# Optimization experiments

Hardware: AMD Instinct MI355X
Metric: run time of the kernel (lower is better)

## Reference

```python
import jax, jax.numpy as jnp
import numpy as np

N_FILTERS = 64
FILTER_SIZE = 64
N_FRAMES = 64
N_TO_KEEP = 128
MIN_SIZE = 512
N_SAMPLES = 32768
BATCH = 8


def pos_encoding(n_elements, n_sinusoids):
    t = np.linspace(1e-8, 1.0, n_elements)
    freq = np.linspace(1e-3, 1.0, n_sinusoids)
    return np.sin(t[:, None] * freq[None, :]).astype(np.float32)


def gammatone_filter_bank(n_filters, size, sr=22050.0):
    # 4th-order gammatone impulse responses, linearly spaced center freqs
    t = np.arange(size) / sr
    freqs = np.linspace(20.0, sr / 2 - 20.0, n_filters)
    b = 1.019 * 24.7 * (4.37 * freqs / 1000.0 + 1.0)  # ERB bandwidths
    g = (t[None, :] ** 3) * np.exp(-2 * np.pi * b[:, None] * t[None, :]) \
        * np.cos(2 * np.pi * freqs[:, None] * t[None, :])
    g = g / (np.abs(g).max(axis=-1, keepdims=True) + 1e-12)
    return g.astype(np.float32)


def setup_inputs() -> dict:
    key = jax.random.key(0)
    k1, k2 = jax.random.split(key)
    return {
        'target': jax.random.normal(k1, (BATCH, 1, N_SAMPLES), dtype=jnp.float32),
        'recon': jax.random.normal(k2, (BATCH, 1, N_SAMPLES), dtype=jnp.float32),
        'filters': jnp.asarray(gammatone_filter_bank(N_FILTERS, FILTER_SIZE)),
        'proj_time': jnp.asarray(pos_encoding(N_FRAMES, 128)),
        'proj_freq': jnp.asarray(pos_encoding(N_FILTERS, 128)),
    }


def fft_frequency_decompose(x, min_size):
    # band-limited octave decomposition: band of size s holds rfft bins [s/4, s/2)
    coeffs = jnp.fft.rfft(x, norm='ortho')
    n = x.shape[-1]
    bands = []
    start, end = 0, min_size // 2
    while end <= n // 2:
        spec = jnp.zeros(x.shape[:-1] + (end + 1,), dtype=coeffs.dtype)
        spec = spec.at[..., start:end].set(coeffs[..., start:end])
        bands.append(jnp.fft.irfft(spec, n=end * 2, norm='ortho'))
        start, end = end, end * 2
    return bands


def fft_convolve(a, b):
    n = a.shape[-1]
    pa = jnp.pad(a, [(0, 0)] * (a.ndim - 1) + [(0, n)])
    pb = jnp.pad(b, [(0, 0)] * (b.ndim - 1) + [(0, n)])
    spec = jnp.fft.rfft(pa) * jnp.fft.rfft(pb)  # broadcasts [B,1,.] x [1,F,.]
    return jnp.fft.irfft(spec, n=2 * n)[..., :n]


def max_pool1d(x, kernel, stride, pad):
    return jax.lax.reduce_window(
        x, -jnp.inf, jax.lax.max,
        (1, 1, kernel), (1, 1, stride),
        [(0, 0), (0, 0), (pad, pad)])


def sparsify2(x, k):
    # top-k over flattened (channels*time); pack events as value-scaled time
    # one-hots and binary channel one-hots
    b, c, t = x.shape
    flat = x.reshape(b, c * t)
    values, indices = jax.lax.top_k(flat, k)  # [b, k]
    ch, tm = indices // t, indices % t
    packed = (tm[..., None] == jnp.arange(t)[None, None, :]).astype(x.dtype) * values[..., None]  # [b,k,t]
    one_hot = (ch[..., None] == jnp.arange(c)[None, None, :]).astype(x.dtype)  # [b,k,c]
    return packed, one_hot


def _feature(x, filters, proj_time, proj_freq):
    bands = fft_frequency_decompose(x, MIN_SIZE)
    outs = []
    for band in bands:  # fixed small set of structurally distinct bands
        samples = band.shape[-1]
        filt = jnp.pad(filters[None, :, :], ((0, 0), (0, 0), (0, samples - FILTER_SIZE)))
        result = fft_convolve(band, filt)  # [B, n_filters, samples]
        stride = samples // 64
        pooled = max_pool1d(result, 2 * stride, stride, stride // 2)[..., :samples]  # [B, 64, 64]
        packed, one_hot = sparsify2(pooled, N_TO_KEEP)
        a = packed @ proj_time   # [B, k, 128]
        b = one_hot @ proj_freq  # [B, k, 128]
        outs.append(jnp.concatenate([a, b], axis=-1))
    return jnp.concatenate(outs, axis=-1)  # [B, k, 256 * n_bands]


def reference(target, recon, filters, proj_time, proj_freq):
    t = _feature(target, filters, proj_time, proj_freq)
    r = _feature(recon, filters, proj_time, proj_freq)
    return jnp.abs(t - r).mean()
```

## Files before the change

kernel.cpp:

```cpp
#include <hip/hip_runtime.h>
#include <hip/hip_bf16.h>

#define N_SAMP    32768
#define NBINS     16384
#define NSIG      16
#define NBANDS    7
#define K_TOP     128
#define BAND_STRIDE 65472

#define SST_F   0
#define SST_PT  4096
#define SST_PF  12288
#define SST_TOT 20480

#define TWO_PI 6.283185307179586f

typedef __attribute__((ext_vector_type(8))) short bf16x8;
typedef __attribute__((ext_vector_type(4))) float f32x4;

__device__ __forceinline__ float bf2f(__hip_bfloat16 v) { return __bfloat162float(v); }

__device__ __forceinline__ unsigned encf(float f) {
    unsigned u = __float_as_uint(f);
    return (u & 0x80000000u) ? ~u : (u | 0x80000000u);
}
__device__ __forceinline__ float decf(unsigned u) {
    return __uint_as_float((u & 0x80000000u) ? (u ^ 0x80000000u) : ~u);
}

__device__ __forceinline__ int band_M1sh(int b) { return b < 3 ? 4 : (b < 4 ? 5 : 6); }
__device__ __forceinline__ int band_Lsh(int b) {
    return b == 0 ? 5 : (b == 1 ? 6 : (b < 5 ? 7 : (b == 5 ? 8 : 9)));
}
__device__ __forceinline__ int band_M2sh(int b) {
    return b < 2 ? 4 : (b < 5 ? 5 : (b == 5 ? 6 : 7));
}

__global__ __launch_bounds__(256) void k_stage(
    const void* __restrict__ t, const void* __restrict__ f,
    const void* __restrict__ pt, const void* __restrict__ pf,
    __hip_bfloat16* __restrict__ staged,
    float* __restrict__ bands, float* __restrict__ accum,
    int* __restrict__ counter)
{
    const int tid = threadIdx.x;
    const int bx  = blockIdx.x;
    if (bx == SST_TOT / 256) {
        for (int i = tid; i < NSIG * 448; i += 256) {
            int sig = i / 448, rem = i - sig * 448;
            int g = rem >> 6, j = rem & 63;
            int off = 64 * g + 512 * ((1 << g) - 1);
            bands[(size_t)sig * BAND_STRIDE + off + j] = 0.f;
        }
        if (tid == 0) { accum[0] = 0.f; counter[0] = 0; }
        return;
    }
    float pv = bf2f(((const __hip_bfloat16*)t)[tid & 63]);
    int bad = (fabsf(pv) > 1e8f) || (pv != pv);
    const int isf32 = (__ballot(bad) != 0ull);
    const int id = bx * 256 + tid;
    const void* src; int idx;
    if (id < SST_PT)      { src = f;  idx = id; }
    else if (id < SST_PF) { src = pt; idx = id - SST_PT; }
    else                  { src = pf; idx = id - SST_PF; }
    float v = isf32 ? ((const float*)src)[idx]
                    : bf2f(((const __hip_bfloat16*)src)[idx]);
    staged[id] = __float2bfloat16(v);
}

__global__ __launch_bounds__(256) void k_fwd1(
    const void* __restrict__ tgt, const void* __restrict__ rec,
    float* __restrict__ T)
{
    const int tid   = threadIdx.x;
    const int sig   = blockIdx.y;
    const int nbase = (blockIdx.x & 1) * 128;
    const int kgrp  = (blockIdx.x >> 1) * 64;
    __shared__ __align__(16) __hip_bfloat16 xT[128][136];
    __shared__ float ct[128], st[128];

    if (tid < 128) {
        float sv, cv;
        sincosf(TWO_PI * (float)tid * (1.f / 128.f), &sv, &cv);
        ct[tid] = cv; st[tid] = sv;
    }

    float pv = bf2f(((const __hip_bfloat16*)tgt)[tid & 63]);
    int bad = (fabsf(pv) > 1e8f) || (pv != pv);
    const int isf32 = (__ballot(bad) != 0ull);
    const void* xsrc = (sig < 8) ? tgt : rec;
    const int soff = (sig & 7) * N_SAMP;

    const int rloc = tid & 127;
    const int chb  = (tid >> 7) * 64;
    for (int c8 = 0; c8 < 64; c8 += 8) {
        union { bf16x8 v; __hip_bfloat16 h[8]; } u;
        #pragma unroll
        for (int uu = 0; uu < 8; ++uu) {
            int n1 = chb + c8 + uu;
            int gi = soff + n1 * 256 + nbase + rloc;
            float xv = isf32 ? ((const float*)xsrc)[gi]
                             : bf2f(((const __hip_bfloat16*)xsrc)[gi]);
            u.h[uu] = __float2bfloat16(xv);
        }
        *(bf16x8*)(&xT[rloc][chb + c8]) = u.v;
    }
    __syncthreads();

    const int tl = tid & 15, quad = (tid >> 4) & 3, w = tid >> 6;
    const int k1 = kgrp + w * 16 + tl;
    bf16x8 Arh[4], Arl[4], Aih[4], Ail[4];
    #pragma unroll
    for (int ki = 0; ki < 4; ++ki) {
        union { bf16x8 v; __hip_bfloat16 h[8]; } rh, rl, ih, il;
        #pragma unroll
        for (int j = 0; j < 8; ++j) {
            int n1 = ki * 32 + quad * 8 + j;
            int tt = (k1 * n1) & 127;
            float wre = ct[tt], wim = -st[tt];
            __hip_bfloat16 h1 = __float2bfloat16(wre);
            rh.h[j] = h1;
            rl.h[j] = __float2bfloat16(wre - bf2f(h1));
            __hip_bfloat16 h2 = __float2bfloat16(wim);
            ih.h[j] = h2;
            il.h[j] = __float2bfloat16(wim - bf2f(h2));
        }
        Arh[ki] = rh.v; Arl[ki] = rl.v; Aih[ki] = ih.v; Ail[ki] = il.v;
    }

    float2* To = (float2*)T + (size_t)sig * 128 * 256;
    const int mk = kgrp + w * 16 + quad * 4;
    for (int ni = 0; ni < 8; ++ni) {
        bf16x8 B[4];
        #pragma unroll
        for (int ki = 0; ki < 4; ++ki)
            B[ki] = *(const bf16x8*)(&xT[ni * 16 + tl][ki * 32 + quad * 8]);
        f32x4 aR = {0.f,0.f,0.f,0.f}, aI = {0.f,0.f,0.f,0.f};
        #pragma unroll
        for (int ki = 0; ki < 4; ++ki) {
            aR = __builtin_amdgcn_mfma_f32_16x16x32_bf16(Arh[ki], B[ki], aR, 0, 0, 0);
            aR = __builtin_amdgcn_mfma_f32_16x16x32_bf16(Arl[ki], B[ki], aR, 0, 0, 0);
            aI = __builtin_amdgcn_mfma_f32_16x16x32_bf16(Aih[ki], B[ki], aI, 0, 0, 0);
            aI = __builtin_amdgcn_mfma_f32_16x16x32_bf16(Ail[ki], B[ki], aI, 0, 0, 0);
        }
        const int n2 = nbase + ni * 16 + tl;
        #pragma unroll
        for (int rg = 0; rg < 4; ++rg) {
            int k1e = mk + rg;
            float sv, cv;
            sincosf((TWO_PI / 32768.f) * (float)(k1e * n2), &sv, &cv);
            float Tr = aR[rg] * cv + aI[rg] * sv;
            float Ti = aI[rg] * cv - aR[rg] * sv;
            To[(size_t)k1e * 256 + n2] = make_float2(Tr, Ti);
        }
    }
}

__global__ __launch_bounds__(128) void k_fwd2(
    const float* __restrict__ T, float* __restrict__ C)
{
    const int k2  = threadIdx.x;
    const int k1  = blockIdx.x;
    const int sig = blockIdx.y;
    __shared__ float2 Ts[256];
    const float2* Tin = (const float2*)T + ((size_t)sig * 128 + k1) * 256;
    for (int i = k2; i < 256; i += 128) Ts[i] = Tin[i];
    __syncthreads();
    float er[4], ei[4];
    #pragma unroll
    for (int c = 0; c < 4; ++c) {
        float sv, cv;
        sincosf(-TWO_PI * (float)((c * k2) & 255) * (1.f / 256.f), &sv, &cv);
        er[c] = cv; ei[c] = sv;
    }
    float s4, c4;
    sincosf(-TWO_PI * (float)((4 * k2) & 255) * (1.f / 256.f), &s4, &c4);
    float Xr[4] = {0.f,0.f,0.f,0.f}, Xi[4] = {0.f,0.f,0.f,0.f};
    for (int n2 = 0; n2 < 256; n2 += 4) {
        #pragma unroll
        for (int c = 0; c < 4; ++c) {
            float2 t = Ts[n2 + c];
            Xr[c] += t.x * er[c] - t.y * ei[c];
            Xi[c] += t.x * ei[c] + t.y * er[c];
            float nr = er[c] * c4 - ei[c] * s4;
            ei[c]    = er[c] * s4 + ei[c] * c4;
            er[c] = nr;
        }
    }
    const float inv = 5.5242717280199030e-3f;
    float xr = (Xr[0] + Xr[1]) + (Xr[2] + Xr[3]);
    float xi = (Xi[0] + Xi[1]) + (Xi[2] + Xi[3]);
    float2* Co = (float2*)C + (size_t)sig * NBINS;
    Co[k1 + 128 * k2] = make_float2(xr * inv, xi * inv);
}

__global__ __launch_bounds__(256) void k_synthA(
    const float* __restrict__ C, float* __restrict__ G)
{
    const int tid = threadIdx.x;
    const int sig = blockIdx.y;
    const int bix = 63 - blockIdx.x;
    const int band = (bix == 0) ? 0 : (32 - __clz(bix));
    const int lbx  = (band == 0) ? 0 : (bix - (1 << (band - 1)));
    const int s    = 512 << band;
    const int m1sh = band_M1sh(band);
    const int lsh  = band_Lsh(band);
    const int m2sh = band_M2sh(band);
    const int M2   = 1 << m2sh;
    const int L    = 1 << lsh;
    const int L4   = L >> 2;
    const int a    = (band == 0) ? 0 : (128 << band);
    const int tix  = lbx * 256 + tid;
    const int j1lo = (lbx * 256) >> (lsh - 2);
    int j1cnt = 256 >> (lsh - 2);
    if (j1cnt > (1 << m1sh)) j1cnt = 1 << m1sh;
    __shared__ float2 Ds[256];
    const float2* D = (const float2*)C + (size_t)sig * NBINS + a;
    for (int i = tid; i < (j1cnt << m2sh); i += 256) {
        int j1o = i >> m2sh, j2 = i & (M2 - 1);
        Ds[i] = D[(j1lo + j1o) + (j2 << m1sh)];
    }
    __syncthreads();
    if (tix >= (128 << band)) return;
    const int j1o = (tix >> (lsh - 2)) - j1lo;
    const int m   = tix & (L4 - 1);
    const float2* Dj = Ds + (j1o << m2sh);
    float e0r = 1.f, e0i = 0.f, e1r, e1i, sr, si;
    sincosf(TWO_PI * (float)m / (float)L, &e1i, &e1r);
    sincosf(TWO_PI * (float)(2 * m) / (float)L, &si, &sr);
    float ar[4] = {0.f,0.f,0.f,0.f}, ai[4] = {0.f,0.f,0.f,0.f};
    for (int j2 = 0; j2 < M2; j2 += 4) {
        {   float2 d = Dj[j2];
            float tr = d.x * e0r - d.y * e0i, ti = d.x * e0i + d.y * e0r;
            ar[0] += tr; ai[0] += ti; ar[1] += tr; ai[1] += ti;
            ar[2] += tr; ai[2] += ti; ar[3] += tr; ai[3] += ti;
            float nr = e0r * sr - e0i * si; e0i = e0r * si + e0i * sr; e0r = nr;
        }
        {   float2 d = Dj[j2 + 1];
            float tr = d.x * e1r - d.y * e1i, ti = d.x * e1i + d.y * e1r;
            ar[0] += tr; ai[0] += ti;
            ar[1] -= ti; ai[1] += tr;
            ar[2] -= tr; ai[2] -= ti;
            ar[3] += ti; ai[3] -= tr;
            float nr = e1r * sr - e1i * si; e1i = e1r * si + e1i * sr; e1r = nr;
        }
        {   float2 d = Dj[j2 + 2];
            float tr = d.x * e0r - d.y * e0i, ti = d.x * e0i + d.y * e0r;
            ar[0] += tr; ai[0] += ti;
            ar[1] -= tr; ai[1] -= ti;
            ar[2] += tr; ai[2] += ti;
            ar[3] -= tr; ai[3] -= ti;
            float nr = e0r * sr - e0i * si; e0i = e0r * si + e0i * sr; e0r = nr;
        }
        {   float2 d = Dj[j2 + 3];
            float tr = d.x * e1r - d.y * e1i, ti = d.x * e1i + d.y * e1r;
            ar[0] += tr; ai[0] += ti;
            ar[1] += ti; ai[1] -= tr;
            ar[2] -= tr; ai[2] -= ti;
            ar[3] -= ti; ai[3] += tr;
            float nr = e1r * sr - e1i * si; e1i = e1r * si + e1i * sr; e1r = nr;
        }
    }
    const float sc = 2.f * rsqrtf((float)s);
    float2* Go = (float2*)G + (size_t)sig * 65024 + 512 * ((1 << band) - 1);
    const int base = ((tix >> (lsh - 2)) << lsh) + m;
    #pragma unroll
    for (int q = 0; q < 4; ++q)
        Go[base + q * L4] = make_float2(ar[q] * sc, ai[q] * sc);
}

__global__ __launch_bounds__(256) void k_synthB(
    const float* __restrict__ C, const float* __restrict__ G,
    float* __restrict__ bands)
{
    const int tid = threadIdx.x;
    const int sig = blockIdx.y;
    const int bix = 63 - blockIdx.x;
    const int band = (bix == 0) ? 0 : (32 - __clz(bix));
    const int lbx  = (band == 0) ? 0 : (bix - (1 << (band - 1)));
    const int s    = 512 << band;
    const int M1   = 1 << band_M1sh(band);
    const int lsh  = band_Lsh(band);
    const int n    = lbx * 256 + tid;
    const int s4   = s >> 2;
    if (n >= s4) return;
    const int m    = n & ((1 << lsh) - 1);
    const float2* Gi = (const float2*)G + (size_t)sig * 65024 + 512 * ((1 << band) - 1);
    float e0r = 1.f, e0i = 0.f, e1r, e1i, sr, si;
    sincosf(TWO_PI * (float)n / (float)s, &e1i, &e1r);
    sincosf(TWO_PI * (float)(2 * n) / (float)s, &si, &sr);
    float zr[4] = {0.f,0.f,0.f,0.f}, zi[4] = {0.f,0.f,0.f,0.f};
    for (int j1 = 0; j1 < M1; j1 += 4) {
        {   float2 g = Gi[((j1 + 0) << lsh) + m];
            float tr = g.x * e0r - g.y * e0i, ti = g.x * e0i + g.y * e0r;
            zr[0] += tr; zi[0] += ti; zr[1] += tr; zi[1] += ti;
            zr[2] += tr; zi[2] += ti; zr[3] += tr; zi[3] += ti;
            float nr = e0r * sr - e0i * si; e0i = e0r * si + e0i * sr; e0r = nr;
        }
        {   float2 g = Gi[((j1 + 1) << lsh) + m];
            float tr = g.x * e1r - g.y * e1i, ti = g.x * e1i + g.y * e1r;
            zr[0] += tr; zi[0] += ti;
            zr[1] -= ti; zi[1] += tr;
            zr[2] -= tr; zi[2] -= ti;
            zr[3] += ti; zi[3] -= tr;
            float nr = e1r * sr - e1i * si; e1i = e1r * si + e1i * sr; e1r = nr;
        }
        {   float2 g = Gi[((j1 + 2) << lsh) + m];
            float tr = g.x * e0r - g.y * e0i, ti = g.x * e0i + g.y * e0r;
            zr[0] += tr; zi[0] += ti;
            zr[1] -= tr; zi[1] -= ti;
            zr[2] += tr; zi[2] += ti;
            zr[3] -= tr; zi[3] -= ti;
            float nr = e0r * sr - e0i * si; e0i = e0r * si + e0i * sr; e0r = nr;
        }
        {   float2 g = Gi[((j1 + 3) << lsh) + m];
            float tr = g.x * e1r - g.y * e1i, ti = g.x * e1i + g.y * e1r;
            zr[0] += tr; zi[0] += ti;
            zr[1] += ti; zi[1] -= tr;
            zr[2] -= tr; zi[2] -= ti;
            zr[3] -= ti; zi[3] += tr;
            float nr = e1r * sr - e1i * si; e1i = e1r * si + e1i * sr; e1r = nr;
        }
    }
    const int poff = 64 * (band + 1) + 512 * ((1 << band) - 1);
    float* bo = bands + (size_t)sig * BAND_STRIDE + poff;
    if (band == 0) {
        const float dc = C[(size_t)sig * NBINS * 2] * 0.04419417382415922f;
        #pragma unroll
        for (int q = 0; q < 4; ++q) bo[n + q * s4] = zr[q] - dc;
    } else {
        #pragma unroll
        for (int q = 0; q < 4; ++q) {
            float val;
            switch (n & 3) {
                case 0:  val =  zr[q]; break;
                case 1:  val = -zi[q]; break;
                case 2:  val = -zr[q]; break;
                default: val =  zi[q]; break;
            }
            bo[n + q * s4] = val;
        }
    }
}

__global__ __launch_bounds__(256) void k_conv(
    const float* __restrict__ bands,
    const __hip_bfloat16* __restrict__ filters,
    float* __restrict__ segG)
{
    const int tid  = threadIdx.x;
    const int sig  = blockIdx.y;
    const int c    = blockIdx.x;
    const int band = 31 - __clz(c + 1);
    const int cidx = c + 1 - (1 << band);
    const int poff = 64 * (band + 1) + 512 * ((1 << band) - 1);
    const float* bp = bands + (size_t)sig * BAND_STRIDE + poff + cidx * 512;

    __shared__ __align__(16) __hip_bfloat16 xr[8][584];
    __shared__ float segP[64 * 4];

    for (int i = tid; i < 576; i += 256) {
        __hip_bfloat16 b = __float2bfloat16(bp[511 - i]);
        #pragma unroll
        for (int p = 0; p < 8; ++p) {
            int idx = i - p;
            if (idx >= 0) xr[p][idx] = b;
        }
    }
    __syncthreads();

    const int tl   = tid & 15;
    const int quad = (tid >> 4) & 3;
    const int wave = tid >> 6;

    bf16x8 bf0[4], bf1[4];
    #pragma unroll
    for (int ft = 0; ft < 4; ++ft) {
        const __hip_bfloat16* fp = filters + ((ft * 16 + tl) * 64 + quad * 8);
        bf0[ft] = *(const bf16x8*)(fp);
        bf1[ft] = *(const bf16x8*)(fp + 32);
    }

    int s0 = 511 - wave * 128 - tl + 8 * quad;
    const __hip_bfloat16* xp = &xr[0][0] + (s0 & 7) * 584 + (s0 & ~7);

    const int spc = 512 >> (2 + band);
    float* segO = segG + (size_t)(sig * NBANDS + band) * 64 * 128 + cidx * spc;

    const float NEG = -3.4e38f;
    float run0 = NEG, run1 = NEG, run2 = NEG, run3 = NEG;
    const int per = (band >= 2) ? (1 << (band - 2)) : 1;

    for (int it = 0; it < 8; ++it) {
        const int t0 = wave * 128 + it * 16;
        bf16x8 a0 = *(const bf16x8*)(xp);
        bf16x8 a1 = *(const bf16x8*)(xp + 32);
        xp -= 16;
        f32x4 ac0 = {0.f,0.f,0.f,0.f}, ac1 = ac0, ac2 = ac0, ac3 = ac0;
        ac0 = __builtin_amdgcn_mfma_f32_16x16x32_bf16(a0, bf0[0], ac0, 0, 0, 0);
        ac0 = __builtin_amdgcn_mfma_f32_16x16x32_bf16(a1, bf1[0], ac0, 0, 0, 0);
        ac1 = __builtin_amdgcn_mfma_f32_16x16x32_bf16(a0, bf0[1], ac1, 0, 0, 0);
        ac1 = __builtin_amdgcn_mfma_f32_16x16x32_bf16(a1, bf1[1], ac1, 0, 0, 0);
        ac2 = __builtin_amdgcn_mfma_f32_16x16x32_bf16(a0, bf0[2], ac2, 0, 0, 0);
        ac2 = __builtin_amdgcn_mfma_f32_16x16x32_bf16(a1, bf1[2], ac2, 0, 0, 0);
        ac3 = __builtin_amdgcn_mfma_f32_16x16x32_bf16(a0, bf0[3], ac3, 0, 0, 0);
        ac3 = __builtin_amdgcn_mfma_f32_16x16x32_bf16(a1, bf1[3], ac3, 0, 0, 0);
        float m0 = fmaxf(fmaxf(ac0[0], ac0[1]), fmaxf(ac0[2], ac0[3]));
        float m1 = fmaxf(fmaxf(ac1[0], ac1[1]), fmaxf(ac1[2], ac1[3]));
        float m2 = fmaxf(fmaxf(ac2[0], ac2[1]), fmaxf(ac2[2], ac2[3]));
        float m3 = fmaxf(fmaxf(ac3[0], ac3[1]), fmaxf(ac3[2], ac3[3]));
        if (band == 0) {
            int sb = (t0 >> 2) + quad;
            segO[(tl     ) * 128 + sb] = m0;
            segO[(tl + 16) * 128 + sb] = m1;
            segO[(tl + 32) * 128 + sb] = m2;
            segO[(tl + 48) * 128 + sb] = m3;
        } else if (band == 1) {
            m0 = fmaxf(m0, __shfl_xor(m0, 16));
            m1 = fmaxf(m1, __shfl_xor(m1, 16));
            m2 = fmaxf(m2, __shfl_xor(m2, 16));
            m3 = fmaxf(m3, __shfl_xor(m3, 16));
            if ((quad & 1) == 0) {
                int sb = (t0 >> 3) + (quad >> 1);
                segO[(tl     ) * 128 + sb] = m0;
                segO[(tl + 16) * 128 + sb] = m1;
                segO[(tl + 32) * 128 + sb] = m2;
                segO[(tl + 48) * 128 + sb] = m3;
            }
        } else {
            m0 = fmaxf(m0, __shfl_xor(m0, 16)); m0 = fmaxf(m0, __shfl_xor(m0, 32));
            m1 = fmaxf(m1, __shfl_xor(m1, 16)); m1 = fmaxf(m1, __shfl_xor(m1, 32));
            m2 = fmaxf(m2, __shfl_xor(m2, 16)); m2 = fmaxf(m2, __shfl_xor(m2, 32));
            m3 = fmaxf(m3, __shfl_xor(m3, 16)); m3 = fmaxf(m3, __shfl_xor(m3, 32));
            run0 = fmaxf(run0, m0); run1 = fmaxf(run1, m1);
            run2 = fmaxf(run2, m2); run3 = fmaxf(run3, m3);
            if (((it + 1) & (per - 1)) == 0) {
                int sb = t0 >> (2 + band);
                float rv = quad == 0 ? run0 : quad == 1 ? run1
                         : quad == 2 ? run2 : run3;
                segO[(tl + 16 * quad) * 128 + sb] = rv;
                run0 = NEG; run1 = NEG; run2 = NEG; run3 = NEG;
            }
        }
    }
    if (band == 6) {
        float rv = quad == 0 ? run0 : quad == 1 ? run1
                 : quad == 2 ? run2 : run3;
        segP[(tl + 16 * quad) * 4 + wave] = rv;
        __syncthreads();
        if (tid < 128) {
            int f = tid & 63, sg = tid >> 6;
            segO[f * 128 + sg] =
                fmaxf(segP[f * 4 + 2 * sg], segP[f * 4 + 2 * sg + 1]);
        }
    }
}

__global__ __launch_bounds__(256) void k_topk(
    const float* __restrict__ segG,
    float* __restrict__ topv, int* __restrict__ topi)
{
    const int tid = threadIdx.x;
    const int band = blockIdx.x, sig = blockIdx.y;
    const float* segB = segG + (size_t)(sig * NBANDS + band) * 64 * 128;

    __shared__ unsigned hist[256];
    __shared__ unsigned scan[256];
    __shared__ unsigned long long list[512];
    __shared__ int sh_B, sh_nA, sh_cnt, sh_num;

    unsigned long long kk[16];
    #pragma unroll
    for (int q = 0; q < 16; ++q) {
        int i = q * 256 + tid;
        int f = i >> 6, t = i & 63;
        const float* sg = segB + f * 128;
        float m = fmaxf(sg[2 * t], sg[2 * t + 1]);
        if (t > 0)  m = fmaxf(m, sg[2 * t - 1]);
        if (t < 63) m = fmaxf(m, sg[2 * t + 2]);
        kk[q] = ((unsigned long long)encf(m) << 32) | (unsigned)(4095 - i);
    }

    int shift = 56;
    unsigned long long prefix = 0;
    int nA = 0;
    for (int lev = 0; lev < 8; ++lev) {
        hist[tid] = 0;
        __syncthreads();
        #pragma unroll
        for (int q = 0; q < 16; ++q) {
            bool inpre = (lev == 0) || ((kk[q] >> (shift + 8)) == prefix);
            if (inpre) atomicAdd(&hist[(unsigned)((kk[q] >> shift) & 255u)], 1u);
        }
        __syncthreads();
        scan[tid] = hist[tid];
        __syncthreads();
        for (int off = 1; off < 256; off <<= 1) {
            unsigned v = scan[tid] + ((tid + off < 256) ? scan[tid + off] : 0u);
            __syncthreads();
            scan[tid] = v;
            __syncthreads();
        }
        {
            unsigned ge = (unsigned)nA + scan[tid];
            unsigned gt = (unsigned)nA + ((tid < 255) ? scan[tid + 1] : 0u);
            if (ge >= 128u && gt < 128u) {
                sh_B = tid; sh_nA = (int)gt; sh_cnt = (int)hist[tid];
            }
        }
        __syncthreads();
        prefix = (prefix << 8) | (unsigned)sh_B;
        nA = sh_nA;
        if (nA + sh_cnt <= 511 || shift == 0) break;
        shift -= 8;
        __syncthreads();
    }

    list[tid] = 0ull; list[tid + 256] = 0ull;
    if (tid == 0) sh_num = 0;
    __syncthreads();
    #pragma unroll
    for (int q = 0; q < 16; ++q) {
        if ((kk[q] >> shift) >= prefix) {
            int p = atomicAdd(&sh_num, 1);
            if (p < 512) list[p] = kk[q];
        }
    }
    __syncthreads();

    for (int k = 2; k <= 512; k <<= 1) {
        for (int j = k >> 1; j > 0; j >>= 1) {
            for (int w = tid; w < 512; w += 256) {
                int l = w ^ j;
                if (l > w) {
                    unsigned long long av = list[w], bv = list[l];
                    bool up = ((w & k) == 0);
                    if ((av > bv) == up) { list[w] = bv; list[l] = av; }
                }
            }
            __syncthreads();
        }
    }
    if (tid < K_TOP) {
        unsigned long long key = list[511 - tid];
        const size_t ob = ((size_t)sig * NBANDS + band) * K_TOP + tid;
        topv[ob] = decf((unsigned)(key >> 32));
        topi[ob] = 4095 - (int)(key & 0xFFFFFFFFu);
    }
}

__global__ __launch_bounds__(256) void k_loss(
    const float* __restrict__ topv, const int* __restrict__ topi,
    const __hip_bfloat16* __restrict__ PT, const __hip_bfloat16* __restrict__ PF,
    float* __restrict__ accum, int* __restrict__ counter,
    unsigned* __restrict__ out)
{
    const int tid = threadIdx.x;
    const int band = blockIdx.x, b = blockIdx.y;
    const size_t bt = ((size_t)b * NBANDS + band) * K_TOP;
    const size_t br = ((size_t)(8 + b) * NBANDS + band) * K_TOP;
    __shared__ float vT[128], vR[128];
    __shared__ int   iT[128], iR[128];
    if (tid < 128) { vT[tid] = topv[bt + tid]; iT[tid] = topi[bt + tid]; }
    else { int j = tid - 128; vR[j] = topv[br + j]; iR[j] = topi[br + j]; }
    __syncthreads();
    float sum = 0.f;
    if (tid < 128) {
        #pragma unroll 4
        for (int k = 0; k < K_TOP; ++k) {
            float a = vT[k] * bf2f(PT[(iT[k] & 63) * 128 + tid]);
            float c = vR[k] * bf2f(PT[(iR[k] & 63) * 128 + tid]);
            sum += fabsf(a - c);
        }
    } else {
        const int j = tid - 128;
        #pragma unroll 4
        for (int k = 0; k < K_TOP; ++k) {
            float a = bf2f(PF[(iT[k] >> 6) * 128 + j]);
            float c = bf2f(PF[(iR[k] >> 6) * 128 + j]);
            sum += fabsf(a - c);
        }
    }
    __shared__ float red[256];
    __shared__ int amLast;
    red[tid] = sum;
    __syncthreads();
    for (int ofs = 128; ofs > 0; ofs >>= 1) {
        if (tid < ofs) red[tid] += red[tid + ofs];
        __syncthreads();
    }
    if (tid == 0) {
        atomicAdd(accum, red[0]);
        __threadfence();
        amLast = (atomicAdd(counter, 1) == NBANDS * 8 - 1);
    }
    __syncthreads();
    if (!amLast) return;
    if (tid == 0) {
        __threadfence();
        float L = atomicAdd(accum, 0.f) * (1.0f / 1835008.0f);
        unsigned lu = __float_as_uint(L);
        bool isnanL = ((lu & 0x7F800000u) == 0x7F800000u) && (lu & 0x007FFFFFu);
        float code;
        if      (isnanL)           code = 500.f;
        else if (L == 0.f)         code = 400.f;
        else if (fabsf(L) < 1e-6f) code = 600.f;
        else                       code = L;
        unsigned fb = __float_as_uint(code);
        unsigned hb = (fb + 0x7FFFu + ((fb >> 16) & 1u)) >> 16;
        out[0] = (hb << 16) | hb;
    }
}

extern "C" void kernel_launch(void* const* d_in, const int* in_sizes, int n_in,
                              void* d_out, int out_size, void* d_ws, size_t ws_size,
                              hipStream_t stream)
{
    float* C      = (float*)d_ws;
    float* bands  = C + (size_t)NSIG * NBINS * 2;
    float* segG   = bands + (size_t)NSIG * BAND_STRIDE;
    float* topv   = segG + (size_t)NSIG * NBANDS * 64 * 128;
    int*   topi   = (int*)(topv + (size_t)NSIG * NBANDS * K_TOP);
    float* accum  = (float*)(topi + (size_t)NSIG * NBANDS * K_TOP);
    int*   counter= (int*)(accum + 1);
    __hip_bfloat16* staged = (__hip_bfloat16*)(accum + 4);
    float* TG = (float*)(staged + SST_TOT);
    float* T  = TG;
    float* G  = TG;

    const __hip_bfloat16* fst = staged + SST_F;
    const __hip_bfloat16* pts = staged + SST_PT;
    const __hip_bfloat16* pfs = staged + SST_PF;

    k_stage  <<<dim3(SST_TOT / 256 + 1), 256, 0, stream>>>(
                 d_in[0], d_in[2], d_in[3], d_in[4], staged, bands, accum, counter);
    k_fwd1   <<<dim3(4, NSIG),       256, 0, stream>>>(d_in[0], d_in[1], T);
    k_fwd2   <<<dim3(128, NSIG),     128, 0, stream>>>(T, C);
    k_synthA <<<dim3(64, NSIG),      256, 0, stream>>>(C, G);
    k_synthB <<<dim3(64, NSIG),      256, 0, stream>>>(C, G, bands);
    k_conv   <<<dim3(127, NSIG),     256, 0, stream>>>(bands, fst, segG);
    k_topk   <<<dim3(NBANDS, NSIG),  256, 0, stream>>>(segG, topv, topi);
    k_loss   <<<dim3(NBANDS, 8),     256, 0, stream>>>(topv, topi, pts, pfs,
                 accum, counter, (unsigned*)d_out);
}
```

Baseline: 208.2 us.

## Replace twiddle sincos with shared tables and use wave-level aggregation in topk

The FFT stage kernels now build shared-memory twiddle tables. The per-element sincosf in k_fwd1 is replaced by a two-level table product (coarse 256-entry times fine 128-entry), and k_fwd2 reads its twiddles from a table. In k_topk, histogram atomics are aggregated per wave using ballot-based peer matching, the block-wide shared-memory suffix scan is replaced by a wave shuffle scan plus a per-wave sum, and list compaction uses a single ballot-aggregated atomic per wave. Together these aim to cut transcendental math, LDS atomic contention and barrier count, at the cost of extra ballots and table-product rounding.

```diff
diff --git a/kernel.cpp b/kernel.cpp
--- a/kernel.cpp
+++ b/kernel.cpp
@@ -78,11 +78,19 @@
     const int kgrp  = (blockIdx.x >> 1) * 64;
     __shared__ __align__(16) __hip_bfloat16 xT[128][136];
     __shared__ float ct[128], st[128];
-
-    if (tid < 128) {
+    __shared__ float2 t256[256];
+    __shared__ float2 tF[128];
+
+    {
         float sv, cv;
-        sincosf(TWO_PI * (float)tid * (1.f / 128.f), &sv, &cv);
-        ct[tid] = cv; st[tid] = sv;
+        sincosf(TWO_PI * (float)tid * (1.f / 256.f), &sv, &cv);
+        t256[tid] = make_float2(cv, -sv);
+        if (tid < 128) {
+            sincosf(TWO_PI * (float)tid * (1.f / 128.f), &sv, &cv);
+            ct[tid] = cv; st[tid] = sv;
+            sincosf(TWO_PI * (float)tid * (1.f / 32768.f), &sv, &cv);
+            tF[tid] = make_float2(cv, -sv);
+        }
     }
 
     float pv = bf2f(((const __hip_bfloat16*)tgt)[tid & 63]);
@@ -147,10 +155,13 @@
         #pragma unroll
         for (int rg = 0; rg < 4; ++rg) {
             int k1e = mk + rg;
-            float sv, cv;
-            sincosf((TWO_PI / 32768.f) * (float)(k1e * n2), &sv, &cv);
-            float Tr = aR[rg] * cv + aI[rg] * sv;
-            float Ti = aI[rg] * cv - aR[rg] * sv;
+            int m = k1e * n2;
+            float2 e1 = t256[m >> 7];
+            float2 e2 = tF[m & 127];
+            float er = e1.x * e2.x - e1.y * e2.y;
+            float ei = e1.x * e2.y + e1.y * e2.x;
+            float Tr = aR[rg] * er - aI[rg] * ei;
+            float Ti = aI[rg] * er + aR[rg] * ei;
             To[(size_t)k1e * 256 + n2] = make_float2(Tr, Ti);
         }
     }
@@ -163,18 +174,24 @@
     const int k1  = blockIdx.x;
     const int sig = blockIdx.y;
     __shared__ float2 Ts[256];
+    __shared__ float2 tw[256];
     const float2* Tin = (const float2*)T + ((size_t)sig * 128 + k1) * 256;
     for (int i = k2; i < 256; i += 128) Ts[i] = Tin[i];
+    {
+        float sv, cv;
+        sincosf(TWO_PI * (float)k2 * (1.f / 256.f), &sv, &cv);
+        tw[k2]       = make_float2(cv, -sv);
+        tw[k2 + 128] = make_float2(-cv, sv);
+    }
     __syncthreads();
     float er[4], ei[4];
     #pragma unroll
     for (int c = 0; c < 4; ++c) {
-        float sv, cv;
-        sincosf(-TWO_PI * (float)((c * k2) & 255) * (1.f / 256.f), &sv, &cv);
-        er[c] = cv; ei[c] = sv;
-    }
-    float s4, c4;
-    sincosf(-TWO_PI * (float)((4 * k2) & 255) * (1.f / 256.f), &s4, &c4);
+        float2 e = tw[(c * k2) & 255];
+        er[c] = e.x; ei[c] = e.y;
+    }
+    float2 e4 = tw[(4 * k2) & 255];
+    const float c4 = e4.x, s4 = e4.y;
     float Xr[4] = {0.f,0.f,0.f,0.f}, Xi[4] = {0.f,0.f,0.f,0.f};
     for (int n2 = 0; n2 < 256; n2 += 4) {
         #pragma unroll
@@ -460,12 +477,14 @@
     const float* __restrict__ segG,
     float* __restrict__ topv, int* __restrict__ topi)
 {
-    const int tid = threadIdx.x;
+    const int tid  = threadIdx.x;
+    const int lane = tid & 63;
+    const int wv   = tid >> 6;
     const int band = blockIdx.x, sig = blockIdx.y;
     const float* segB = segG + (size_t)(sig * NBANDS + band) * 64 * 128;
 
     __shared__ unsigned hist[256];
-    __shared__ unsigned scan[256];
+    __shared__ unsigned wsum[4];
     __shared__ unsigned long long list[512];
     __shared__ int sh_B, sh_nA, sh_cnt, sh_num;
 
@@ -485,28 +504,38 @@
     unsigned long long prefix = 0;
     int nA = 0;
     for (int lev = 0; lev < 8; ++lev) {
-        hist[tid] = 0;
+        hist[tid] = 0u;
         __syncthreads();
         #pragma unroll
         for (int q = 0; q < 16; ++q) {
             bool inpre = (lev == 0) || ((kk[q] >> (shift + 8)) == prefix);
-            if (inpre) atomicAdd(&hist[(unsigned)((kk[q] >> shift) & 255u)], 1u);
+            unsigned b = (unsigned)((kk[q] >> shift) & 255u);
+            unsigned long long peers = __ballot(inpre);
+            #pragma unroll
+            for (int bit = 0; bit < 8; ++bit) {
+                unsigned long long bm = __ballot((b >> bit) & 1u);
+                peers &= ((b >> bit) & 1u) ? bm : ~bm;
+            }
+            if (inpre && (peers & ((1ull << lane) - 1ull)) == 0ull)
+                atomicAdd(&hist[b], (unsigned)__builtin_popcountll(peers));
         }
         __syncthreads();
-        scan[tid] = hist[tid];
+        unsigned hcnt = hist[tid];
+        unsigned sfx = hcnt;
+        #pragma unroll
+        for (int off = 1; off < 64; off <<= 1) {
+            unsigned o = __shfl_down(sfx, off);
+            sfx += (lane + off < 64) ? o : 0u;
+        }
+        if (lane == 0) wsum[wv] = sfx;
         __syncthreads();
-        for (int off = 1; off < 256; off <<= 1) {
-            unsigned v = scan[tid] + ((tid + off < 256) ? scan[tid + off] : 0u);
-            __syncthreads();
-            scan[tid] = v;
-            __syncthreads();
-        }
-        {
-            unsigned ge = (unsigned)nA + scan[tid];
-            unsigned gt = (unsigned)nA + ((tid < 255) ? scan[tid + 1] : 0u);
-            if (ge >= 128u && gt < 128u) {
-                sh_B = tid; sh_nA = (int)gt; sh_cnt = (int)hist[tid];
-            }
+        unsigned addhi = 0u;
+        #pragma unroll
+        for (int w2 = 1; w2 < 4; ++w2) addhi += (w2 > wv) ? wsum[w2] : 0u;
+        unsigned ge = (unsigned)nA + sfx + addhi;
+        unsigned gt = ge - hcnt;
+        if (ge >= 128u && gt < 128u) {
+            sh_B = tid; sh_nA = (int)gt; sh_cnt = (int)hcnt;
         }
         __syncthreads();
         prefix = (prefix << 8) | (unsigned)sh_B;
@@ -521,9 +550,17 @@
     __syncthreads();
     #pragma unroll
     for (int q = 0; q < 16; ++q) {
-        if ((kk[q] >> shift) >= prefix) {
-            int p = atomicAdd(&sh_num, 1);
-            if (p < 512) list[p] = kk[q];
+        bool sel = (kk[q] >> shift) >= prefix;
+        unsigned long long m = __ballot(sel);
+        if (m != 0ull) {
+            int lead = __builtin_ctzll(m);
+            int base = 0;
+            if (lane == lead) base = atomicAdd(&sh_num, __builtin_popcountll(m));
+            base = __shfl(base, lead);
+            if (sel) {
+                int p = base + __builtin_popcountll(m & ((1ull << lane) - 1ull));
+                if (p < 512) list[p] = kk[q];
+            }
         }
     }
     __syncthreads();
```

New measurement: 213.5 us. 1.03x slower.

## Fuse staging into fwd1, chain topk and loss into conv via last-block counters

Applied to the files above, without the earlier changes.

The staging and zero-init work moves into an extra block column of k_fwd1, and the separate k_topk and k_loss kernels are folded into the tail of k_conv. Per-band and per-pair atomic counters elect the last finishing block to run top-k and then the loss. Per-element sincosf twiddles in fwd1 and fwd2 are replaced by small shared-memory lookup tables. This removes three kernel launches and their gaps, at the cost of more shared memory in k_conv, serialized tail work on the elected blocks, and fence-based cross-block ordering.

```diff
diff --git a/kernel.cpp b/kernel.cpp
--- a/kernel.cpp
+++ b/kernel.cpp
@@ -36,53 +36,64 @@
     return b < 2 ? 4 : (b < 5 ? 5 : (b == 5 ? 6 : 7));
 }
 
-__global__ __launch_bounds__(256) void k_stage(
-    const void* __restrict__ t, const void* __restrict__ f,
-    const void* __restrict__ pt, const void* __restrict__ pf,
+__global__ __launch_bounds__(256) void k_fwd1(
+    const void* __restrict__ tgt, const void* __restrict__ rec,
+    const void* __restrict__ f, const void* __restrict__ pt,
+    const void* __restrict__ pf,
     __hip_bfloat16* __restrict__ staged,
     float* __restrict__ bands, float* __restrict__ accum,
-    int* __restrict__ counter)
-{
-    const int tid = threadIdx.x;
-    const int bx  = blockIdx.x;
-    if (bx == SST_TOT / 256) {
-        for (int i = tid; i < NSIG * 448; i += 256) {
-            int sig = i / 448, rem = i - sig * 448;
-            int g = rem >> 6, j = rem & 63;
-            int off = 64 * g + 512 * ((1 << g) - 1);
-            bands[(size_t)sig * BAND_STRIDE + off + j] = 0.f;
-        }
-        if (tid == 0) { accum[0] = 0.f; counter[0] = 0; }
-        return;
-    }
-    float pv = bf2f(((const __hip_bfloat16*)t)[tid & 63]);
-    int bad = (fabsf(pv) > 1e8f) || (pv != pv);
-    const int isf32 = (__ballot(bad) != 0ull);
-    const int id = bx * 256 + tid;
-    const void* src; int idx;
-    if (id < SST_PT)      { src = f;  idx = id; }
-    else if (id < SST_PF) { src = pt; idx = id - SST_PT; }
-    else                  { src = pf; idx = id - SST_PF; }
-    float v = isf32 ? ((const float*)src)[idx]
-                    : bf2f(((const __hip_bfloat16*)src)[idx]);
-    staged[id] = __float2bfloat16(v);
-}
-
-__global__ __launch_bounds__(256) void k_fwd1(
-    const void* __restrict__ tgt, const void* __restrict__ rec,
+    int* __restrict__ counter, int* __restrict__ bandCnt,
+    int* __restrict__ lossCnt,
     float* __restrict__ T)
 {
     const int tid   = threadIdx.x;
     const int sig   = blockIdx.y;
+
+    if (blockIdx.x == 4) {
+        float pv0 = bf2f(((const __hip_bfloat16*)tgt)[tid & 63]);
+        int bad0 = (fabsf(pv0) > 1e8f) || (pv0 != pv0);
+        const int isf = (__ballot(bad0) != 0ull);
+        #pragma unroll
+        for (int k = 0; k < 5; ++k) {
+            int id = sig * 1280 + k * 256 + tid;
+            const void* src; int idx;
+            if (id < SST_PT)      { src = f;  idx = id; }
+            else if (id < SST_PF) { src = pt; idx = id - SST_PT; }
+            else                  { src = pf; idx = id - SST_PF; }
+            float v = isf ? ((const float*)src)[idx]
+                          : bf2f(((const __hip_bfloat16*)src)[idx]);
+            staged[id] = __float2bfloat16(v);
+        }
+        for (int i = tid; i < 448; i += 256) {
+            int g = i >> 6, j = i & 63;
+            int off = 64 * g + 512 * ((1 << g) - 1);
+            bands[(size_t)sig * BAND_STRIDE + off + j] = 0.f;
+        }
+        if (sig == 0) {
+            if (tid == 0) { accum[0] = 0.f; counter[0] = 0; }
+            if (tid < NSIG * NBANDS) bandCnt[tid] = 0;
+            if (tid >= 128 && tid < 128 + 8 * NBANDS) lossCnt[tid - 128] = 0;
+        }
+        return;
+    }
+
     const int nbase = (blockIdx.x & 1) * 128;
     const int kgrp  = (blockIdx.x >> 1) * 64;
     __shared__ __align__(16) __hip_bfloat16 xT[128][136];
     __shared__ float ct[128], st[128];
-
-    if (tid < 128) {
+    __shared__ float2 t256[256];
+    __shared__ float2 tF[128];
+
+    {
         float sv, cv;
-        sincosf(TWO_PI * (float)tid * (1.f / 128.f), &sv, &cv);
-        ct[tid] = cv; st[tid] = sv;
+        sincosf(TWO_PI * (float)tid * (1.f / 256.f), &sv, &cv);
+        t256[tid] = make_float2(cv, -sv);
+        if (tid < 128) {
+            sincosf(TWO_PI * (float)tid * (1.f / 128.f), &sv, &cv);
+            ct[tid] = cv; st[tid] = sv;
+            sincosf(TWO_PI * (float)tid * (1.f / 32768.f), &sv, &cv);
+            tF[tid] = make_float2(cv, -sv);
+        }
     }
 
     float pv = bf2f(((const __hip_bfloat16*)tgt)[tid & 63]);
@@ -147,10 +158,13 @@
         #pragma unroll
         for (int rg = 0; rg < 4; ++rg) {
             int k1e = mk + rg;
-            float sv, cv;
-            sincosf((TWO_PI / 32768.f) * (float)(k1e * n2), &sv, &cv);
-            float Tr = aR[rg] * cv + aI[rg] * sv;
-            float Ti = aI[rg] * cv - aR[rg] * sv;
+            int m = k1e * n2;
+            float2 e1 = t256[m >> 7];
+            float2 e2 = tF[m & 127];
+            float er = e1.x * e2.x - e1.y * e2.y;
+            float ei = e1.x * e2.y + e1.y * e2.x;
+            float Tr = aR[rg] * er - aI[rg] * ei;
+            float Ti = aI[rg] * er + aR[rg] * ei;
             To[(size_t)k1e * 256 + n2] = make_float2(Tr, Ti);
         }
     }
@@ -163,18 +177,24 @@
     const int k1  = blockIdx.x;
     const int sig = blockIdx.y;
     __shared__ float2 Ts[256];
+    __shared__ float2 tw[256];
     const float2* Tin = (const float2*)T + ((size_t)sig * 128 + k1) * 256;
     for (int i = k2; i < 256; i += 128) Ts[i] = Tin[i];
+    {
+        float sv, cv;
+        sincosf(TWO_PI * (float)k2 * (1.f / 256.f), &sv, &cv);
+        tw[k2]       = make_float2(cv, -sv);
+        tw[k2 + 128] = make_float2(-cv, sv);
+    }
     __syncthreads();
     float er[4], ei[4];
     #pragma unroll
     for (int c = 0; c < 4; ++c) {
-        float sv, cv;
-        sincosf(-TWO_PI * (float)((c * k2) & 255) * (1.f / 256.f), &sv, &cv);
-        er[c] = cv; ei[c] = sv;
-    }
-    float s4, c4;
-    sincosf(-TWO_PI * (float)((4 * k2) & 255) * (1.f / 256.f), &s4, &c4);
+        float2 e = tw[(c * k2) & 255];
+        er[c] = e.x; ei[c] = e.y;
+    }
+    float2 e4 = tw[(4 * k2) & 255];
+    const float c4 = e4.x, s4 = e4.y;
     float Xr[4] = {0.f,0.f,0.f,0.f}, Xi[4] = {0.f,0.f,0.f,0.f};
     for (int n2 = 0; n2 < 256; n2 += 4) {
         #pragma unroll
@@ -346,7 +366,12 @@
 __global__ __launch_bounds__(256) void k_conv(
     const float* __restrict__ bands,
     const __hip_bfloat16* __restrict__ filters,
-    float* __restrict__ segG)
+    float* __restrict__ segG,
+    float* __restrict__ topv, int* __restrict__ topi,
+    const __hip_bfloat16* __restrict__ PT, const __hip_bfloat16* __restrict__ PF,
+    int* __restrict__ bandCnt, int* __restrict__ lossCnt,
+    float* __restrict__ accum, int* __restrict__ counter,
+    unsigned* __restrict__ out)
 {
     const int tid  = threadIdx.x;
     const int sig  = blockIdx.y;
@@ -358,6 +383,14 @@
 
     __shared__ __align__(16) __hip_bfloat16 xr[8][584];
     __shared__ float segP[64 * 4];
+    __shared__ unsigned hist[256];
+    __shared__ unsigned scan[256];
+    __shared__ unsigned long long list[512];
+    __shared__ int sh_B, sh_nA, sh_cnt, sh_num;
+    __shared__ float vT[128], vR[128];
+    __shared__ int   iT[128], iR[128];
+    __shared__ float red[256];
+    __shared__ int amLast, sh_win, sh_w2;
 
     for (int i = tid; i < 576; i += 256) {
         __hip_bfloat16 b = __float2bfloat16(bp[511 - i]);
@@ -454,21 +487,17 @@
                 fmaxf(segP[f * 4 + 2 * sg], segP[f * 4 + 2 * sg + 1]);
         }
     }
-}
-
-__global__ __launch_bounds__(256) void k_topk(
-    const float* __restrict__ segG,
-    float* __restrict__ topv, int* __restrict__ topi)
-{
-    const int tid = threadIdx.x;
-    const int band = blockIdx.x, sig = blockIdx.y;
+
+    __syncthreads();
+    if (tid == 0) {
+        __threadfence();
+        sh_win = (atomicAdd(&bandCnt[sig * NBANDS + band], 1) == (1 << band) - 1);
+    }
+    __syncthreads();
+    if (!sh_win) return;
+    __threadfence();
+
     const float* segB = segG + (size_t)(sig * NBANDS + band) * 64 * 128;
-
-    __shared__ unsigned hist[256];
-    __shared__ unsigned scan[256];
-    __shared__ unsigned long long list[512];
-    __shared__ int sh_B, sh_nA, sh_cnt, sh_num;
-
     unsigned long long kk[16];
     #pragma unroll
     for (int q = 0; q < 16; ++q) {
@@ -547,20 +576,19 @@
         topv[ob] = decf((unsigned)(key >> 32));
         topi[ob] = 4095 - (int)(key & 0xFFFFFFFFu);
     }
-}
-
-__global__ __launch_bounds__(256) void k_loss(
-    const float* __restrict__ topv, const int* __restrict__ topi,
-    const __hip_bfloat16* __restrict__ PT, const __hip_bfloat16* __restrict__ PF,
-    float* __restrict__ accum, int* __restrict__ counter,
-    unsigned* __restrict__ out)
-{
-    const int tid = threadIdx.x;
-    const int band = blockIdx.x, b = blockIdx.y;
+
+    __syncthreads();
+    if (tid == 0) {
+        __threadfence();
+        sh_w2 = (atomicAdd(&lossCnt[(sig & 7) * NBANDS + band], 1) == 1);
+    }
+    __syncthreads();
+    if (!sh_w2) return;
+    __threadfence();
+
+    const int b = sig & 7;
     const size_t bt = ((size_t)b * NBANDS + band) * K_TOP;
     const size_t br = ((size_t)(8 + b) * NBANDS + band) * K_TOP;
-    __shared__ float vT[128], vR[128];
-    __shared__ int   iT[128], iR[128];
     if (tid < 128) { vT[tid] = topv[bt + tid]; iT[tid] = topi[bt + tid]; }
     else { int j = tid - 128; vR[j] = topv[br + j]; iR[j] = topi[br + j]; }
     __syncthreads();
@@ -569,20 +597,18 @@
         #pragma unroll 4
         for (int k = 0; k < K_TOP; ++k) {
             float a = vT[k] * bf2f(PT[(iT[k] & 63) * 128 + tid]);
-            float c = vR[k] * bf2f(PT[(iR[k] & 63) * 128 + tid]);
-            sum += fabsf(a - c);
+            float cc = vR[k] * bf2f(PT[(iR[k] & 63) * 128 + tid]);
+            sum += fabsf(a - cc);
         }
     } else {
         const int j = tid - 128;
         #pragma unroll 4
         for (int k = 0; k < K_TOP; ++k) {
             float a = bf2f(PF[(iT[k] >> 6) * 128 + j]);
-            float c = bf2f(PF[(iR[k] >> 6) * 128 + j]);
-            sum += fabsf(a - c);
-        }
-    }
-    __shared__ float red[256];
-    __shared__ int amLast;
+            float cc = bf2f(PF[(iR[k] >> 6) * 128 + j]);
+            sum += fabsf(a - cc);
+        }
+    }
     red[tid] = sum;
     __syncthreads();
     for (int ofs = 128; ofs > 0; ofs >>= 1) {
@@ -623,7 +649,9 @@
     int*   topi   = (int*)(topv + (size_t)NSIG * NBANDS * K_TOP);
     float* accum  = (float*)(topi + (size_t)NSIG * NBANDS * K_TOP);
     int*   counter= (int*)(accum + 1);
-    __hip_bfloat16* staged = (__hip_bfloat16*)(accum + 4);
+    int*   bandCnt= (int*)(accum + 4);
+    int*   lossCnt= bandCnt + NSIG * NBANDS;
+    __hip_bfloat16* staged = (__hip_bfloat16*)(accum + 172);
     float* TG = (float*)(staged + SST_TOT);
     float* T  = TG;
     float* G  = TG;
@@ -632,14 +660,13 @@
     const __hip_bfloat16* pts = staged + SST_PT;
     const __hip_bfloat16* pfs = staged + SST_PF;
 
-    k_stage  <<<dim3(SST_TOT / 256 + 1), 256, 0, stream>>>(
-                 d_in[0], d_in[2], d_in[3], d_in[4], staged, bands, accum, counter);
-    k_fwd1   <<<dim3(4, NSIG),       256, 0, stream>>>(d_in[0], d_in[1], T);
-    k_fwd2   <<<dim3(128, NSIG),     128, 0, stream>>>(T, C);
-    k_synthA <<<dim3(64, NSIG),      256, 0, stream>>>(C, G);
-    k_synthB <<<dim3(64, NSIG),      256, 0, stream>>>(C, G, bands);
-    k_conv   <<<dim3(127, NSIG),     256, 0, stream>>>(bands, fst, segG);
-    k_topk   <<<dim3(NBANDS, NSIG),  256, 0, stream>>>(segG, topv, topi);
-    k_loss   <<<dim3(NBANDS, 8),     256, 0, stream>>>(topv, topi, pts, pfs,
-                 accum, counter, (unsigned*)d_out);
-}
+    k_fwd1   <<<dim3(5, NSIG),   256, 0, stream>>>(d_in[0], d_in[1],
+                 d_in[2], d_in[3], d_in[4], staged, bands, accum, counter,
+                 bandCnt, lossCnt, T);
+    k_fwd2   <<<dim3(128, NSIG), 128, 0, stream>>>(T, C);
+    k_synthA <<<dim3(64, NSIG),  256, 0, stream>>>(C, G);
+    k_synthB <<<dim3(64, NSIG),  256, 0, stream>>>(C, G, bands);
+    k_conv   <<<dim3(127, NSIG), 256, 0, stream>>>(bands, fst, segG,
+                 topv, topi, pts, pfs, bandCnt, lossCnt, accum, counter,
+                 (unsigned*)d_out);
+}
```

New measurement: 339.3 us. 1.63x slower.
